# Kernel optimization log

Hardware: AMD Instinct MI355X
Metric: run time of the kernel (lower is better)

## Reference

```python
import jax, jax.numpy as jnp
import numpy as np
import math

# ---- static configuration (matches init_kwargs) ----
METADATA = [64, 48, 32]   # channels per l = 0,1,2
MAX_L = 3                 # order_out
N_BATCH = 32768
fact = math.factorial

def _cg_complex(l1, m1, l2, m2, l3, m3):
    # Clebsch-Gordan coefficient <l1 m1 l2 m2 | l3 m3> via Racah formula
    if m1 + m2 != m3 or l3 < abs(l1 - l2) or l3 > l1 + l2:
        return 0.0
    pre = math.sqrt((2*l3+1) * fact(l1+l2-l3) * fact(l1-l2+l3) * fact(-l1+l2+l3) / fact(l1+l2+l3+1))
    pre *= math.sqrt(fact(l1+m1)*fact(l1-m1)*fact(l2+m2)*fact(l2-m2)*fact(l3+m3)*fact(l3-m3))
    kmin = max(0, l2-l3-m1, l1-l3+m2)
    kmax = min(l1+l2-l3, l1-m1, l2+m2)
    s = 0.0
    for k in range(kmin, kmax+1):
        s += (-1)**k / (fact(k)*fact(l1+l2-l3-k)*fact(l1-m1-k)*fact(l2+m2-k)*fact(l3-l2+m1+k)*fact(l3-l1-m2+k))
    return pre * s

def _U(l):
    # complex->real spherical harmonic change of basis, rows = real m', cols = complex m
    U = np.zeros((2*l+1, 2*l+1), dtype=np.complex128)
    for m in range(-l, l+1):
        r = m + l
        if m > 0:
            U[r, m+l] = (-1)**m / math.sqrt(2.0); U[r, -m+l] = 1.0/math.sqrt(2.0)
        elif m == 0:
            U[r, l] = 1.0
        else:
            U[r, m+l] = 1j/math.sqrt(2.0); U[r, -m+l] = -1j*(-1)**m/math.sqrt(2.0)
    return U

def _real_cg(l1, l2, l3):
    Cc = np.zeros((2*l1+1, 2*l2+1, 2*l3+1))
    for m1 in range(-l1, l1+1):
        for m2 in range(-l2, l2+1):
            for m3 in range(-l3, l3+1):
                Cc[m1+l1, m2+l2, m3+l3] = _cg_complex(l1, m1, l2, m2, l3, m3)
    T = np.einsum('am,bn,co,mno->abc', _U(l1), _U(l2), _U(l3).conj(), Cc.astype(np.complex128))
    T = T.imag if np.abs(T.imag).max() > np.abs(T.real).max() else T.real
    return np.ascontiguousarray(T).astype(np.float32)

# ---- static index structures ----
L_IN = len(METADATA)
OFF_IN = np.concatenate([[0], np.cumsum([METADATA[l]*(2*l+1) for l in range(L_IN)])]).astype(np.int64)
DIM_IN = int(OFF_IN[-1])  # 368
PATHS = []
for l1 in range(L_IN):
    for l2 in range(L_IN):
        for l3 in range(abs(l1-l2), min(l1+l2, MAX_L)+1):
            PATHS.append((l1, l2, l3, min(METADATA[l1], METADATA[l2])))
MD_OV = [0]*(MAX_L+1)
for (_, _, l3, ch) in PATHS:
    MD_OV[l3] = max(MD_OV[l3], ch)
OFF_OUT = np.concatenate([[0], np.cumsum([MD_OV[l]*(2*l+1) for l in range(MAX_L+1)])]).astype(np.int64)
DIM_OUT = int(OFF_OUT[-1])  # 672
CG = {(l1, l2, l3): jnp.asarray(_real_cg(l1, l2, l3)) for (l1, l2, l3, _) in PATHS}

_mix_id, _scat = [], []
_base = 0
for (l1, l2, l3, ch) in PATHS:
    for i in range(ch):
        for m in range(2*l3+1):
            _mix_id.append(_base + i)
            _scat.append(int(OFF_OUT[l3]) + i*(2*l3+1) + m)
    _base += ch
MIX_ID = jnp.asarray(np.array(_mix_id, dtype=np.int64))
SCATTER = jnp.asarray(np.array(_scat, dtype=np.int64))
N_MIX = _base  # 688

_chan_in = []
_cb = 0
for l in range(L_IN):
    for i in range(METADATA[l]):
        _chan_in += [_cb + i]*(2*l+1)
    _cb += METADATA[l]
CHAN_IN = jnp.asarray(np.array(_chan_in, dtype=np.int64))
N_KEEP = _cb  # 144
_kin, _kout = [], []
for l in range(L_IN):
    cp = min(METADATA[l], MD_OV[l])
    for i in range(cp):
        for m in range(2*l+1):
            _kin.append(int(OFF_IN[l]) + i*(2*l+1) + m)
            _kout.append(int(OFF_OUT[l]) + i*(2*l+1) + m)
KEEP_IN = jnp.asarray(np.array(_kin, dtype=np.int64))
KEEP_OUT = jnp.asarray(np.array(_kout, dtype=np.int64))

SQ3 = math.sqrt(3.0)

def setup_inputs() -> dict:
    key = jax.random.key(0)
    k1, k2, k3 = jax.random.split(key, 3)
    x = jax.random.normal(k1, (N_BATCH, DIM_IN), dtype=jnp.float32)
    keep_coeff = jax.random.uniform(k2, (N_KEEP,), minval=-SQ3, maxval=SQ3, dtype=jnp.float32)
    mix_coeff = jax.random.uniform(k3, (N_MIX,), minval=-SQ3, maxval=SQ3, dtype=jnp.float32)
    return {"x": x, "keep_coeff": keep_coeff, "mix_coeff": mix_coeff}

def reference(x, keep_coeff, mix_coeff):
    n = x.shape[0]
    # keep path: per-channel coeff broadcast over m components
    x_keep = x * keep_coeff[CHAN_IN]  # [N, 368]
    # CG tensor-product self-coupling (diagonal channel pairing per path)
    tps = []
    for (l1, l2, l3, ch) in PATHS:
        x1 = x[:, OFF_IN[l1]:OFF_IN[l1]+ch*(2*l1+1)].reshape(n, ch, 2*l1+1)
        x2 = x[:, OFF_IN[l2]:OFF_IN[l2]+ch*(2*l2+1)].reshape(n, ch, 2*l2+1)
        tps.append(jnp.einsum('nia,nib,abm->nim', x1, x2, CG[(l1, l2, l3)]).reshape(n, -1))
    cat = jnp.concatenate(tps, axis=1)  # [N, 2576] non-overlapped TP output
    cat = cat * 0.5 * mix_coeff[MIX_ID]
    # scatter (index_add) into overlapped output layout
    out = jnp.zeros((n, DIM_OUT), dtype=x.dtype).at[:, SCATTER].add(cat)
    # gather + add of keep path (index_select + add_)
    out = out.at[:, KEEP_OUT].add(x_keep[:, KEEP_IN])
    return out
```

## Files before the change

kernel.cpp:

```cpp
#include <hip/hip_runtime.h>


namespace cgc {

struct cplx { double re, im; };
constexpr cplx cmul(cplx a, cplx b){ return {a.re*b.re - a.im*b.im, a.re*b.im + a.im*b.re}; }

constexpr double cfact(int n){ double r = 1.0; for (int i = 2; i <= n; ++i) r *= i; return r; }
constexpr double cabsd(double x){ return x < 0 ? -x : x; }

constexpr double csqrtd(double x){
  if (x <= 0.0) return 0.0;
  double g = x > 1.0 ? x : 1.0;
  for (int i = 0; i < 48; ++i) g = 0.5*(g + x/g);
  return g;
}

constexpr double SQRT2 = csqrtd(2.0);

constexpr double cg_complex(int l1,int m1,int l2,int m2,int l3,int m3){
  if (m1 + m2 != m3) return 0.0;
  int lo = l1 > l2 ? l1 - l2 : l2 - l1;
  if (l3 < lo || l3 > l1 + l2) return 0.0;
  double pre = csqrtd((2*l3+1) * cfact(l1+l2-l3)*cfact(l1-l2+l3)*cfact(-l1+l2+l3)/cfact(l1+l2+l3+1));
  pre *= csqrtd(cfact(l1+m1)*cfact(l1-m1)*cfact(l2+m2)*cfact(l2-m2)*cfact(l3+m3)*cfact(l3-m3));
  int kmin = 0;
  if (l2-l3-m1 > kmin) kmin = l2-l3-m1;
  if (l1-l3+m2 > kmin) kmin = l1-l3+m2;
  int kmax = l1+l2-l3;
  if (l1-m1 < kmax) kmax = l1-m1;
  if (l2+m2 < kmax) kmax = l2+m2;
  double s = 0.0;
  for (int k = kmin; k <= kmax; ++k){
    double d = cfact(k)*cfact(l1+l2-l3-k)*cfact(l1-m1-k)*cfact(l2+m2-k)
             * cfact(l3-l2+m1+k)*cfact(l3-l1-m2+k);
    s += ((k & 1) ? -1.0 : 1.0) / d;
  }
  return pre * s;
}

constexpr cplx Uent(int l, int r, int c){
  int m = r - l;
  if (m > 0){
    if (c ==  m + l) return { ((m & 1) ? -1.0 : 1.0)/SQRT2, 0.0 };
    if (c == -m + l) return { 1.0/SQRT2, 0.0 };
    return {0.0, 0.0};
  } else if (m == 0){
    if (c == l) return {1.0, 0.0};
    return {0.0, 0.0};
  } else {
    int ma = -m;
    if (c ==  m + l) return { 0.0, 1.0/SQRT2 };
    if (c == -m + l) return { 0.0, -(((ma & 1) ? -1.0 : 1.0))/SQRT2 };
    return {0.0, 0.0};
  }
}

template<int L1,int L2,int L3>
struct CGData { float w[(2*L1+1)*(2*L2+1)*(2*L3+1)]; };

template<int L1,int L2,int L3>
constexpr CGData<L1,L2,L3> make_cg(){
  constexpr int D1 = 2*L1+1, D2 = 2*L2+1, D3 = 2*L3+1;
  cplx U1[D1*D1] = {}; cplx U2[D2*D2] = {}; cplx U3c[D3*D3] = {};
  for (int r = 0; r < D1; ++r) for (int c = 0; c < D1; ++c) U1[r*D1+c] = Uent(L1, r, c);
  for (int r = 0; r < D2; ++r) for (int c = 0; c < D2; ++c) U2[r*D2+c] = Uent(L2, r, c);
  for (int r = 0; r < D3; ++r) for (int c = 0; c < D3; ++c){
    cplx u = Uent(L3, r, c); u.im = -u.im; U3c[r*D3+c] = u;
  }
  double Cc[D1*D2*D3] = {};
  for (int m1 = -L1; m1 <= L1; ++m1)
    for (int m2 = -L2; m2 <= L2; ++m2){
      int m3 = m1 + m2;
      if (m3 < -L3 || m3 > L3) continue;
      Cc[((m1+L1)*D2 + (m2+L2))*D3 + (m3+L3)] = cg_complex(L1,m1,L2,m2,L3,m3);
    }
  double re[D1*D2*D3] = {}; double im[D1*D2*D3] = {};
  for (int a = 0; a < D1; ++a)
    for (int b = 0; b < D2; ++b)
      for (int c = 0; c < D3; ++c){
        double sre = 0.0, sim = 0.0;
        for (int m = 0; m < D1; ++m)
          for (int n = 0; n < D2; ++n){
            int o = m + n - L1 - L2 + L3;
            if (o < 0 || o >= D3) continue;
            double cc = Cc[(m*D2+n)*D3 + o];
            if (cc == 0.0) continue;
            cplx p = cmul(cmul(U1[a*D1+m], U2[b*D2+n]), U3c[c*D3+o]);
            sre += p.re * cc; sim += p.im * cc;
          }
        re[(a*D2+b)*D3+c] = sre; im[(a*D2+b)*D3+c] = sim;
      }
  double mre = 0.0, mim = 0.0;
  for (int k = 0; k < D1*D2*D3; ++k){
    if (cabsd(re[k]) > mre) mre = cabsd(re[k]);
    if (cabsd(im[k]) > mim) mim = cabsd(im[k]);
  }
  CGData<L1,L2,L3> outv{};
  for (int k = 0; k < D1*D2*D3; ++k){
    double v = (mim > mre) ? im[k] : re[k];
    outv.w[k] = (cabsd(v) < 1e-10) ? 0.0f : (float)v;
  }
  return outv;
}

}

template<int L1,int L2,int L3>
__device__ __forceinline__ void tp_path(const float* xa, const float* xb, float cmix, float* acc){
  constexpr cgc::CGData<L1,L2,L3> cg = cgc::make_cg<L1,L2,L3>();
  constexpr int D1 = 2*L1+1, D2 = 2*L2+1, D3 = 2*L3+1;
  #pragma unroll
  for (int a = 0; a < D1; ++a){
    #pragma unroll
    for (int b = 0; b < D2; ++b){
      const float pr = xa[a] * xb[b];
      #pragma unroll
      for (int m = 0; m < D3; ++m){
        const float W = cg.w[(a*D2+b)*D3 + m];
        if (W != 0.0f) acc[m] += (cmix * W) * pr;
      }
    }
  }
}


constexpr int RPB      = 4;
constexpr int IN_DIM   = 368;
constexpr int OUT_DIM  = 672;
constexpr int OUT_PAD  = 676;

__global__ __launch_bounds__(256, 4) void selfmix_kernel(
    const float* __restrict__ x, const float* __restrict__ keep,
    const float* __restrict__ mix, float* __restrict__ out, int n)
{
  __shared__ float sout[RPB * OUT_PAD];

  const int tid  = threadIdx.x;
  const int rb   = blockIdx.x * RPB;
  const int rows = (n - rb < RPB) ? (n - rb) : RPB;

  if (tid < 128){
    const int row = tid >> 5;
    const int i   = tid & 31;
    if (row < rows){
      const float* xr = x + (size_t)(rb + row) * IN_DIM;
      float*     orow = sout + row * OUT_PAD;
      const float s = xr[i];
      float p[3], d[5];
      #pragma unroll
      for (int k = 0; k < 3; ++k) p[k] = xr[64 + i*3 + k];
      #pragma unroll
      for (int k = 0; k < 5; ++k) d[k] = xr[208 + i*5 + k];

      float o0 = 0.f;
      float o1[3] = {0.f,0.f,0.f};
      float o2[5] = {0.f,0.f,0.f,0.f,0.f};
      float o3[7] = {0.f,0.f,0.f,0.f,0.f,0.f,0.f};

      tp_path<0,0,0>(&s,&s, 0.5f*mix[  0+i], &o0);
      tp_path<0,1,1>(&s, p, 0.5f*mix[ 64+i],  o1);
      tp_path<0,2,2>(&s, d, 0.5f*mix[112+i],  o2);
      tp_path<1,0,1>( p,&s, 0.5f*mix[144+i],  o1);
      tp_path<1,1,0>( p, p, 0.5f*mix[192+i], &o0);
      tp_path<1,1,1>( p, p, 0.5f*mix[240+i],  o1);
      tp_path<1,1,2>( p, p, 0.5f*mix[288+i],  o2);
      tp_path<1,2,1>( p, d, 0.5f*mix[336+i],  o1);
      tp_path<1,2,2>( p, d, 0.5f*mix[368+i],  o2);
      tp_path<1,2,3>( p, d, 0.5f*mix[400+i],  o3);
      tp_path<2,0,2>( d,&s, 0.5f*mix[432+i],  o2);
      tp_path<2,1,1>( d, p, 0.5f*mix[464+i],  o1);
      tp_path<2,1,2>( d, p, 0.5f*mix[496+i],  o2);
      tp_path<2,1,3>( d, p, 0.5f*mix[528+i],  o3);
      tp_path<2,2,0>( d, d, 0.5f*mix[560+i], &o0);
      tp_path<2,2,1>( d, d, 0.5f*mix[592+i],  o1);
      tp_path<2,2,2>( d, d, 0.5f*mix[624+i],  o2);
      tp_path<2,2,3>( d, d, 0.5f*mix[656+i],  o3);

      o0 += keep[i] * s;
      const float k1 = keep[64+i], k2 = keep[112+i];
      #pragma unroll
      for (int k = 0; k < 3; ++k) o1[k] += k1 * p[k];
      #pragma unroll
      for (int k = 0; k < 5; ++k) o2[k] += k2 * d[k];

      orow[i] = o0;
      #pragma unroll
      for (int k = 0; k < 3; ++k) orow[ 64 + i*3 + k] = o1[k];
      #pragma unroll
      for (int k = 0; k < 5; ++k) orow[208 + i*5 + k] = o2[k];
      #pragma unroll
      for (int k = 0; k < 7; ++k) orow[448 + i*7 + k] = o3[k];
    }
  } else if (tid < 192){
    const int u   = tid - 128;
    const int row = u >> 4;
    const int i   = 32 + (u & 15);
    if (row < rows){
      const float* xr = x + (size_t)(rb + row) * IN_DIM;
      float*     orow = sout + row * OUT_PAD;
      const float s = xr[i];
      float p[3];
      #pragma unroll
      for (int k = 0; k < 3; ++k) p[k] = xr[64 + i*3 + k];

      float o0 = 0.f;
      float o1[3] = {0.f,0.f,0.f};
      float o2[5] = {0.f,0.f,0.f,0.f,0.f};

      tp_path<0,0,0>(&s,&s, 0.5f*mix[  0+i], &o0);
      tp_path<0,1,1>(&s, p, 0.5f*mix[ 64+i],  o1);
      tp_path<1,0,1>( p,&s, 0.5f*mix[144+i],  o1);
      tp_path<1,1,0>( p, p, 0.5f*mix[192+i], &o0);
      tp_path<1,1,1>( p, p, 0.5f*mix[240+i],  o1);
      tp_path<1,1,2>( p, p, 0.5f*mix[288+i],  o2);

      o0 += keep[i] * s;
      const float k1 = keep[64+i];
      #pragma unroll
      for (int k = 0; k < 3; ++k) o1[k] += k1 * p[k];

      orow[i] = o0;
      #pragma unroll
      for (int k = 0; k < 3; ++k) orow[ 64 + i*3 + k] = o1[k];
      #pragma unroll
      for (int k = 0; k < 5; ++k) orow[208 + i*5 + k] = o2[k];
    }
  } else {
    const int u   = tid - 192;
    const int row = u >> 4;
    const int i   = 48 + (u & 15);
    if (row < rows){
      const float s = x[(size_t)(rb + row) * IN_DIM + i];
      float o0 = 0.f;
      tp_path<0,0,0>(&s,&s, 0.5f*mix[0+i], &o0);
      o0 += keep[i] * s;
      sout[row * OUT_PAD + i] = o0;
    }
  }
  __syncthreads();

  {
    float4* gout = (float4*)(out + (size_t)rb * OUT_DIM);
    const float4* so4 = (const float4*)sout;
    const int nf4 = rows * (OUT_DIM / 4);
    for (int t = tid; t < nf4; t += 256){
      const int r = t / 168;
      const int j = t - r * 168;
      gout[t] = so4[r * 169 + j];
    }
  }
}

extern "C" void kernel_launch(void* const* d_in, const int* in_sizes, int n_in,
                              void* d_out, int out_size, void* d_ws, size_t ws_size,
                              hipStream_t stream)
{
  const float* x    = (const float*)d_in[0];
  const float* keep = (const float*)d_in[1];
  const float* mix  = (const float*)d_in[2];
  float* out = (float*)d_out;
  const int n = in_sizes[0] / IN_DIM;
  const int blocks = (n + RPB - 1) / RPB;
  selfmix_kernel<<<blocks, 256, 0, stream>>>(x, keep, mix, out, n);
}
```

Before: 146.7 us.

## Make kernel persistent with register prefetch of next tile and hoisted coefficients

Switches from one block per 4-row tile to a fixed grid of 1024 blocks, each looping over a contiguous range of tiles. The mix and keep coefficients are loaded once per thread into registers, and the next tile's inputs are prefetched into registers while the current tile is computed. LDS barriers become a custom waitcnt plus s_barrier. This removes per-block launch and coefficient reload overhead and overlaps global loads with compute, at the cost of more registers and two barriers per tile. Fewer resident blocks may also reduce latency hiding.

Result: slower. 265.4 us (+80.9%).

```diff
diff --git a/kernel.cpp b/kernel.cpp
--- a/kernel.cpp
+++ b/kernel.cpp
@@ -124,11 +124,16 @@
   }
 }
 
+__device__ __forceinline__ void sync_lds(){
+  asm volatile("s_waitcnt lgkmcnt(0)\n\ts_barrier" ::: "memory");
+}
+
 
 constexpr int RPB      = 4;
 constexpr int IN_DIM   = 368;
 constexpr int OUT_DIM  = 672;
 constexpr int OUT_PAD  = 676;
+constexpr int NBLK     = 1024;
 
 __global__ __launch_bounds__(256, 4) void selfmix_kernel(
     const float* __restrict__ x, const float* __restrict__ keep,
@@ -136,119 +141,176 @@
 {
   __shared__ float sout[RPB * OUT_PAD];
 
-  const int tid  = threadIdx.x;
-  const int rb   = blockIdx.x * RPB;
-  const int rows = (n - rb < RPB) ? (n - rb) : RPB;
-
-  if (tid < 128){
-    const int row = tid >> 5;
-    const int i   = tid & 31;
-    if (row < rows){
-      const float* xr = x + (size_t)(rb + row) * IN_DIM;
-      float*     orow = sout + row * OUT_PAD;
-      const float s = xr[i];
-      float p[3], d[5];
-      #pragma unroll
-      for (int k = 0; k < 3; ++k) p[k] = xr[64 + i*3 + k];
-      #pragma unroll
-      for (int k = 0; k < 5; ++k) d[k] = xr[208 + i*5 + k];
-
-      float o0 = 0.f;
-      float o1[3] = {0.f,0.f,0.f};
-      float o2[5] = {0.f,0.f,0.f,0.f,0.f};
-      float o3[7] = {0.f,0.f,0.f,0.f,0.f,0.f,0.f};
-
-      tp_path<0,0,0>(&s,&s, 0.5f*mix[  0+i], &o0);
-      tp_path<0,1,1>(&s, p, 0.5f*mix[ 64+i],  o1);
-      tp_path<0,2,2>(&s, d, 0.5f*mix[112+i],  o2);
-      tp_path<1,0,1>( p,&s, 0.5f*mix[144+i],  o1);
-      tp_path<1,1,0>( p, p, 0.5f*mix[192+i], &o0);
-      tp_path<1,1,1>( p, p, 0.5f*mix[240+i],  o1);
-      tp_path<1,1,2>( p, p, 0.5f*mix[288+i],  o2);
-      tp_path<1,2,1>( p, d, 0.5f*mix[336+i],  o1);
-      tp_path<1,2,2>( p, d, 0.5f*mix[368+i],  o2);
-      tp_path<1,2,3>( p, d, 0.5f*mix[400+i],  o3);
-      tp_path<2,0,2>( d,&s, 0.5f*mix[432+i],  o2);
-      tp_path<2,1,1>( d, p, 0.5f*mix[464+i],  o1);
-      tp_path<2,1,2>( d, p, 0.5f*mix[496+i],  o2);
-      tp_path<2,1,3>( d, p, 0.5f*mix[528+i],  o3);
-      tp_path<2,2,0>( d, d, 0.5f*mix[560+i], &o0);
-      tp_path<2,2,1>( d, d, 0.5f*mix[592+i],  o1);
-      tp_path<2,2,2>( d, d, 0.5f*mix[624+i],  o2);
-      tp_path<2,2,3>( d, d, 0.5f*mix[656+i],  o3);
-
-      o0 += keep[i] * s;
-      const float k1 = keep[64+i], k2 = keep[112+i];
-      #pragma unroll
-      for (int k = 0; k < 3; ++k) o1[k] += k1 * p[k];
-      #pragma unroll
-      for (int k = 0; k < 5; ++k) o2[k] += k2 * d[k];
-
-      orow[i] = o0;
-      #pragma unroll
-      for (int k = 0; k < 3; ++k) orow[ 64 + i*3 + k] = o1[k];
-      #pragma unroll
-      for (int k = 0; k < 5; ++k) orow[208 + i*5 + k] = o2[k];
-      #pragma unroll
-      for (int k = 0; k < 7; ++k) orow[448 + i*7 + k] = o3[k];
-    }
-  } else if (tid < 192){
-    const int u   = tid - 128;
-    const int row = u >> 4;
-    const int i   = 32 + (u & 15);
-    if (row < rows){
-      const float* xr = x + (size_t)(rb + row) * IN_DIM;
-      float*     orow = sout + row * OUT_PAD;
-      const float s = xr[i];
-      float p[3];
-      #pragma unroll
-      for (int k = 0; k < 3; ++k) p[k] = xr[64 + i*3 + k];
-
-      float o0 = 0.f;
-      float o1[3] = {0.f,0.f,0.f};
-      float o2[5] = {0.f,0.f,0.f,0.f,0.f};
-
-      tp_path<0,0,0>(&s,&s, 0.5f*mix[  0+i], &o0);
-      tp_path<0,1,1>(&s, p, 0.5f*mix[ 64+i],  o1);
-      tp_path<1,0,1>( p,&s, 0.5f*mix[144+i],  o1);
-      tp_path<1,1,0>( p, p, 0.5f*mix[192+i], &o0);
-      tp_path<1,1,1>( p, p, 0.5f*mix[240+i],  o1);
-      tp_path<1,1,2>( p, p, 0.5f*mix[288+i],  o2);
-
-      o0 += keep[i] * s;
-      const float k1 = keep[64+i];
-      #pragma unroll
-      for (int k = 0; k < 3; ++k) o1[k] += k1 * p[k];
-
-      orow[i] = o0;
-      #pragma unroll
-      for (int k = 0; k < 3; ++k) orow[ 64 + i*3 + k] = o1[k];
-      #pragma unroll
-      for (int k = 0; k < 5; ++k) orow[208 + i*5 + k] = o2[k];
-    }
+  const int tid    = threadIdx.x;
+  const int ntiles = (n + RPB - 1) / RPB;
+  const int per    = (ntiles + NBLK - 1) / NBLK;
+  const int tbeg   = blockIdx.x * per;
+  const int tend   = (tbeg + per < ntiles) ? (tbeg + per) : ntiles;
+  if (tbeg >= ntiles) return;
+
+  int row, i, cls;
+  if (tid < 128){ cls = 0; row = tid >> 5;        i = tid & 31; }
+  else if (tid < 192){ cls = 1; row = (tid-128) >> 4; i = 32 + ((tid-128) & 15); }
+  else { cls = 2; row = (tid-192) >> 4; i = 48 + ((tid-192) & 15); }
+
+  float cf[21];
+  #pragma unroll
+  for (int k = 0; k < 21; ++k) cf[k] = 0.f;
+  if (cls == 0){
+    cf[ 0]=0.5f*mix[    i]; cf[ 1]=0.5f*mix[ 64+i]; cf[ 2]=0.5f*mix[112+i];
+    cf[ 3]=0.5f*mix[144+i]; cf[ 4]=0.5f*mix[192+i]; cf[ 5]=0.5f*mix[240+i];
+    cf[ 6]=0.5f*mix[288+i]; cf[ 7]=0.5f*mix[336+i]; cf[ 8]=0.5f*mix[368+i];
+    cf[ 9]=0.5f*mix[400+i]; cf[10]=0.5f*mix[432+i]; cf[11]=0.5f*mix[464+i];
+    cf[12]=0.5f*mix[496+i]; cf[13]=0.5f*mix[528+i]; cf[14]=0.5f*mix[560+i];
+    cf[15]=0.5f*mix[592+i]; cf[16]=0.5f*mix[624+i]; cf[17]=0.5f*mix[656+i];
+    cf[18]=keep[i]; cf[19]=keep[64+i]; cf[20]=keep[112+i];
+  } else if (cls == 1){
+    cf[0]=0.5f*mix[    i]; cf[1]=0.5f*mix[ 64+i]; cf[2]=0.5f*mix[144+i];
+    cf[3]=0.5f*mix[192+i]; cf[4]=0.5f*mix[240+i]; cf[5]=0.5f*mix[288+i];
+    cf[6]=keep[i]; cf[7]=keep[64+i];
   } else {
-    const int u   = tid - 192;
-    const int row = u >> 4;
-    const int i   = 48 + (u & 15);
-    if (row < rows){
-      const float s = x[(size_t)(rb + row) * IN_DIM + i];
-      float o0 = 0.f;
-      tp_path<0,0,0>(&s,&s, 0.5f*mix[0+i], &o0);
-      o0 += keep[i] * s;
-      sout[row * OUT_PAD + i] = o0;
-    }
-  }
-  __syncthreads();
+    cf[0]=0.5f*mix[i]; cf[1]=keep[i];
+  }
+
+  float cin[9], nin[9];
+  #pragma unroll
+  for (int k = 0; k < 9; ++k){ cin[k] = 0.f; nin[k] = 0.f; }
 
   {
-    float4* gout = (float4*)(out + (size_t)rb * OUT_DIM);
-    const float4* so4 = (const float4*)sout;
-    const int nf4 = rows * (OUT_DIM / 4);
-    for (int t = tid; t < nf4; t += 256){
-      const int r = t / 168;
-      const int j = t - r * 168;
-      gout[t] = so4[r * 169 + j];
-    }
+    const int r0 = tbeg * RPB + row;
+    if (r0 < n){
+      const float* xr = x + (size_t)r0 * IN_DIM;
+      cin[0] = xr[i];
+      if (cls <= 1){
+        #pragma unroll
+        for (int k = 0; k < 3; ++k) cin[1+k] = xr[64 + i*3 + k];
+      }
+      if (cls == 0){
+        #pragma unroll
+        for (int k = 0; k < 5; ++k) cin[4+k] = xr[208 + i*5 + k];
+      }
+    }
+  }
+
+  for (int t = tbeg; t < tend; ++t){
+    const int rb   = t * RPB;
+    const int rows = (n - rb < RPB) ? (n - rb) : RPB;
+
+    if (t + 1 < tend){
+      const int r1 = (t+1) * RPB + row;
+      if (r1 < n){
+        const float* xr = x + (size_t)r1 * IN_DIM;
+        nin[0] = xr[i];
+        if (cls <= 1){
+          #pragma unroll
+          for (int k = 0; k < 3; ++k) nin[1+k] = xr[64 + i*3 + k];
+        }
+        if (cls == 0){
+          #pragma unroll
+          for (int k = 0; k < 5; ++k) nin[4+k] = xr[208 + i*5 + k];
+        }
+      }
+    }
+
+    if (cls == 0){
+      if (row < rows){
+        const float s = cin[0];
+        const float* p = &cin[1];
+        const float* d = &cin[4];
+        float* orow = sout + row * OUT_PAD;
+
+        float o0 = 0.f;
+        float o1[3] = {0.f,0.f,0.f};
+        float o2[5] = {0.f,0.f,0.f,0.f,0.f};
+        float o3[7] = {0.f,0.f,0.f,0.f,0.f,0.f,0.f};
+
+        tp_path<0,0,0>(&s,&s, cf[ 0], &o0);
+        tp_path<0,1,1>(&s, p, cf[ 1],  o1);
+        tp_path<0,2,2>(&s, d, cf[ 2],  o2);
+        tp_path<1,0,1>( p,&s, cf[ 3],  o1);
+        tp_path<1,1,0>( p, p, cf[ 4], &o0);
+        tp_path<1,1,1>( p, p, cf[ 5],  o1);
+        tp_path<1,1,2>( p, p, cf[ 6],  o2);
+        tp_path<1,2,1>( p, d, cf[ 7],  o1);
+        tp_path<1,2,2>( p, d, cf[ 8],  o2);
+        tp_path<1,2,3>( p, d, cf[ 9],  o3);
+        tp_path<2,0,2>( d,&s, cf[10],  o2);
+        tp_path<2,1,1>( d, p, cf[11],  o1);
+        tp_path<2,1,2>( d, p, cf[12],  o2);
+        tp_path<2,1,3>( d, p, cf[13],  o3);
+        tp_path<2,2,0>( d, d, cf[14], &o0);
+        tp_path<2,2,1>( d, d, cf[15],  o1);
+        tp_path<2,2,2>( d, d, cf[16],  o2);
+        tp_path<2,2,3>( d, d, cf[17],  o3);
+
+        o0 += cf[18] * s;
+        #pragma unroll
+        for (int k = 0; k < 3; ++k) o1[k] += cf[19] * p[k];
+        #pragma unroll
+        for (int k = 0; k < 5; ++k) o2[k] += cf[20] * d[k];
+
+        orow[i] = o0;
+        #pragma unroll
+        for (int k = 0; k < 3; ++k) orow[ 64 + i*3 + k] = o1[k];
+        #pragma unroll
+        for (int k = 0; k < 5; ++k) orow[208 + i*5 + k] = o2[k];
+        #pragma unroll
+        for (int k = 0; k < 7; ++k) orow[448 + i*7 + k] = o3[k];
+      }
+    } else if (cls == 1){
+      if (row < rows){
+        const float s = cin[0];
+        const float* p = &cin[1];
+        float* orow = sout + row * OUT_PAD;
+
+        float o0 = 0.f;
+        float o1[3] = {0.f,0.f,0.f};
+        float o2[5] = {0.f,0.f,0.f,0.f,0.f};
+
+        tp_path<0,0,0>(&s,&s, cf[0], &o0);
+        tp_path<0,1,1>(&s, p, cf[1],  o1);
+        tp_path<1,0,1>( p,&s, cf[2],  o1);
+        tp_path<1,1,0>( p, p, cf[3], &o0);
+        tp_path<1,1,1>( p, p, cf[4],  o1);
+        tp_path<1,1,2>( p, p, cf[5],  o2);
+
+        o0 += cf[6] * s;
+        #pragma unroll
+        for (int k = 0; k < 3; ++k) o1[k] += cf[7] * p[k];
+
+        orow[i] = o0;
+        #pragma unroll
+        for (int k = 0; k < 3; ++k) orow[ 64 + i*3 + k] = o1[k];
+        #pragma unroll
+        for (int k = 0; k < 5; ++k) orow[208 + i*5 + k] = o2[k];
+      }
+    } else {
+      if (row < rows){
+        const float s = cin[0];
+        float o0 = 0.f;
+        tp_path<0,0,0>(&s,&s, cf[0], &o0);
+        o0 += cf[1] * s;
+        sout[row * OUT_PAD + i] = o0;
+      }
+    }
+
+    sync_lds();
+
+    {
+      float4* gout = (float4*)(out + (size_t)rb * OUT_DIM);
+      const float4* so4 = (const float4*)sout;
+      const int nf4 = rows * (OUT_DIM / 4);
+      for (int q = tid; q < nf4; q += 256){
+        const int r = q / 168;
+        const int j = q - r * 168;
+        gout[q] = so4[r * 169 + j];
+      }
+    }
+
+    sync_lds();
+
+    #pragma unroll
+    for (int k = 0; k < 9; ++k) cin[k] = nin[k];
   }
 }
 
@@ -261,6 +323,5 @@
   const float* mix  = (const float*)d_in[2];
   float* out = (float*)d_out;
   const int n = in_sizes[0] / IN_DIM;
-  const int blocks = (n + RPB - 1) / RPB;
-  selfmix_kernel<<<blocks, 256, 0, stream>>>(x, keep, mix, out, n);
-}
+  selfmix_kernel<<<NBLK, 256, 0, stream>>>(x, keep, mix, out, n);
+}
```
